# Performance work log

Hardware: AMD Instinct MI355X
Metric: run time of the kernel (lower is better)

The kernel has to match this reference:

```python
import jax, jax.numpy as jnp
from jax import lax
import numpy as np


def setup_inputs() -> dict:
    key = jax.random.key(0)
    ks = jax.random.split(key, 9)
    B, L, Dm = 2, 2048, 768
    di, ds, dc = 1536, 16, 4
    def w(k, shape, fan_in):
        return jax.random.normal(k, shape, jnp.float32) / np.sqrt(fan_in)
    return {
        "x": jax.random.normal(ks[0], (B, L, Dm), jnp.float32),
        "W_in": w(ks[1], (2 * di, Dm), Dm),
        "W_conv": w(ks[2], (di, 1, dc), dc),          # depthwise conv kernel (torch layout)
        "W_x": w(ks[3], (2 * ds, di), di),
        "W_dt": w(ks[4], (di, di), di),
        "b_dt": jax.random.normal(ks[5], (di,), jnp.float32) * 0.1,
        "A_log": jnp.log(jnp.arange(1, ds + 1, dtype=jnp.float32)),
        "D": jnp.ones((di,), jnp.float32),
        "W_out": w(ks[6], (Dm, di), di),
    }


def reference(x, W_in, W_conv, W_x, W_dt, b_dt, A_log, D, W_out):
    B, L, Dm = x.shape
    di = W_in.shape[0] // 2
    ds = A_log.shape[0]
    dc = W_conv.shape[-1]

    xz = x @ W_in.T                                   # (B,L,2*di)
    x_part, z = xz[..., :di], xz[..., di:]

    # causal depthwise conv1d (torch pads dc-1 both sides then truncates -> left pad only)
    xc = lax.conv_general_dilated(
        x_part.transpose(0, 2, 1), W_conv, window_strides=(1,),
        padding=[(dc - 1, 0)], feature_group_count=di)  # (B,di,L)
    xc = jax.nn.silu(xc.transpose(0, 2, 1))            # (B,L,di)

    A = -jnp.exp(A_log)                                # (ds,)
    x_dbl = xc @ W_x.T                                 # (B,L,2*ds)
    B_ssm, C_ssm = x_dbl[..., :ds], x_dbl[..., ds:]
    delta = jax.nn.softplus(xc @ W_dt.T + b_dt)        # (B,L,di)

    deltaA = jnp.exp(delta[..., None] * A)             # (B,L,di,ds)
    deltaB = delta[..., None] * B_ssm[:, :, None, :]   # (B,L,di,ds)

    def step(h, inp):
        dA_t, dB_t, C_t = inp                          # (B,di,ds),(B,di,ds),(B,ds)
        h = dA_t * h + dB_t
        y = jnp.einsum('bds,bs->bd', h, C_t)
        return h, y

    h0 = jnp.zeros((B, di, ds), x.dtype)
    _, ys = lax.scan(step, h0, (deltaA.transpose(1, 0, 2, 3),
                                deltaB.transpose(1, 0, 2, 3),
                                C_ssm.transpose(1, 0, 2)))
    y = ys.transpose(1, 0, 2) + D * xc                 # (B,L,di)
    y = y * jax.nn.silu(z)
    return y @ W_out.T                                 # (B,L,Dm)
```

## Files before the change

### kernel.cpp

```cpp
#include <hip/hip_runtime.h>
#include <hip/hip_bf16.h>

#define BB 2
#define LL 2048
#define DM 768
#define DI 1536
#define DS 16
#define MM (BB*LL)
#define NCH 32
#define CHL 64
#define SEQS (BB*DI*DS)
#define NC2 1664

typedef __hip_bfloat16 bf16;
typedef short bf16x8 __attribute__((ext_vector_type(8)));
typedef float f32x4  __attribute__((ext_vector_type(4)));

__device__ __forceinline__ void gl_lds16(const void* g, void* l) {
  __builtin_amdgcn_global_load_lds((const __attribute__((address_space(1))) void*)g,
                                   (__attribute__((address_space(3))) void*)l, 16, 0, 0);
}

struct bf4 { __hip_bfloat16 a, b, c, d; };
#define PR0 786432
#define PR1 589824
#define PR2 294912
#define PR3 638976
#define PRTOT (PR0+PR1+PR2+PR3)

__global__ __launch_bounds__(256) void prep_k(const float* __restrict__ x,
                                              const float* __restrict__ Win,
                                              const float* __restrict__ Wout,
                                              const float* __restrict__ Wdt,
                                              const float* __restrict__ Wx,
                                              __hip_bfloat16* __restrict__ xbf,
                                              __hip_bfloat16* __restrict__ Winbf,
                                              __hip_bfloat16* __restrict__ Woutbf,
                                              __hip_bfloat16* __restrict__ Wcomb) {
  int i = blockIdx.x * 256 + threadIdx.x;
  if (i >= PRTOT) return;
  float4 v; __hip_bfloat16* dst; int di_;
  if (i < PR0)                    { v = ((const float4*)x)[i];                 dst = xbf;    di_ = i; }
  else if (i < PR0 + PR1)         { di_ = i - PR0; v = ((const float4*)Win)[di_];  dst = Winbf; }
  else if (i < PR0 + PR1 + PR2)   { di_ = i - PR0 - PR1; v = ((const float4*)Wout)[di_]; dst = Woutbf; }
  else {
    di_ = i - PR0 - PR1 - PR2;
    int e = di_ * 4, row = e / DI, colb = e % DI;
    if (row < DI)            v = ((const float4*)Wdt)[di_];
    else if (row < DI + 32)  v = *(const float4*)(Wx + (size_t)(row - DI) * DI + colb);
    else                     v = make_float4(0.f, 0.f, 0.f, 0.f);
    dst = Wcomb;
  }
  bf4 o = { __float2bfloat16(v.x), __float2bfloat16(v.y),
            __float2bfloat16(v.z), __float2bfloat16(v.w) };
  ((bf4*)dst)[di_] = o;
}

template<int EPI, int BM>
__global__ __launch_bounds__(256) void gemm_db(const bf16* __restrict__ A,
                                               const bf16* __restrict__ W,
                                               void* __restrict__ Cv,
                                               void* __restrict__ C2v,
                                               const float* __restrict__ bias,
                                               int M, int N, int K) {
  constexpr int NA  = BM / 64;
  constexpr int NPW = NA + 2;
  __shared__ short sA[3][BM * 32];
  __shared__ short sB[3][128 * 32];
  const int t = threadIdx.x;
  const int m0 = blockIdx.y * BM, n0 = blockIdx.x * 128;
  const int w = t >> 6, lane = t & 63;
  const int wm = (w >> 1) * (BM / 2), wn = (w & 1) * 64;
  const int ga = wm >> 4, gb = wn >> 4;

  f32x4 acc[BM / 32][4] = {};

  const int srow = lane & 15, skoff = (lane >> 4) * 8;
  const bf16* gA[NA]; const bf16* gB[2];
  #pragma unroll
  for (int j = 0; j < NA; j++)
    gA[j] = A + (size_t)(m0 + (w + 4 * j) * 16 + srow) * K + skoff;
  #pragma unroll
  for (int j = 0; j < 2; j++)
    gB[j] = W + (size_t)(n0 + (w + 4 * j) * 16 + srow) * K + skoff;

  #define ISSUE(buf, k0)                                              \
    do {                                                              \
      _Pragma("unroll")                                               \
      for (int j = 0; j < NA; j++)                                    \
        gl_lds16(gA[j] + (k0), &sA[buf][(w + 4 * j) * 512]);          \
      _Pragma("unroll")                                               \
      for (int j = 0; j < 2; j++)                                     \
        gl_lds16(gB[j] + (k0), &sB[buf][(w + 4 * j) * 512]);          \
    } while (0)

  ISSUE(0, 0);
  ISSUE(1, 32);
  int p = 0;
  for (int k0 = 0; k0 < K; k0 += 32) {
    if (k0 + 32 < K) {
      asm volatile("s_waitcnt vmcnt(%0)\n\ts_barrier" :: "n"(NPW) : "memory");
    } else {
      asm volatile("s_waitcnt vmcnt(0)\n\ts_barrier" ::: "memory");
    }
    if (k0 + 64 < K) {
      int nb = p + 2; if (nb >= 3) nb -= 3;
      ISSUE(nb, k0 + 64);
    }
    const bf16x8* fA = (const bf16x8*)sA[p];
    const bf16x8* fB = (const bf16x8*)sB[p];
    bf16x8 af[BM / 32], bfr[4];
    #pragma unroll
    for (int i = 0; i < BM / 32; i++) af[i]  = fA[(ga + i) * 64 + lane];
    #pragma unroll
    for (int j = 0; j < 4; j++)       bfr[j] = fB[(gb + j) * 64 + lane];
    #pragma unroll
    for (int i = 0; i < BM / 32; i++)
      #pragma unroll
      for (int j = 0; j < 4; j++)
        acc[i][j] = __builtin_amdgcn_mfma_f32_16x16x32_bf16(af[i], bfr[j], acc[i][j], 0, 0, 0);
    p++; if (p >= 3) p = 0;
  }
  #undef ISSUE

  const int q = lane >> 4, mm = lane & 15;
  #pragma unroll
  for (int i = 0; i < BM / 32; i++)
    #pragma unroll
    for (int j = 0; j < 4; j++) {
      int r0  = m0 + wm + i * 16 + q * 4;
      int col = n0 + wn + j * 16 + mm;
      #pragma unroll
      for (int r = 0; r < 4; r++) {
        float v = acc[i][j][r];
        if (EPI == 0) {
          ((float*)Cv)[(size_t)(r0 + r) * N + col] = v;
        } else if (EPI == 5) {
          if (col < DI) ((bf16*)Cv) [(size_t)(r0 + r) * DI + col]        = __float2bfloat16(v);
          else          ((bf16*)C2v)[(size_t)(r0 + r) * DI + (col - DI)] = __float2bfloat16(v);
        } else {
          if (col < DI) {
            float vv = v + bias[col];
            vv = (vv > 15.f) ? vv : __logf(1.f + __expf(vv));
            ((bf16*)Cv)[(size_t)(r0 + r) * DI + col] = __float2bfloat16(vv);
          } else if (col < DI + 32) {
            ((float*)C2v)[(size_t)(r0 + r) * 32 + (col - DI)] = v;
          }
        }
      }
    }
}

__global__ __launch_bounds__(256) void conv_silu_k(const bf16* __restrict__ xpart,
                                                   const float* __restrict__ Wc,
                                                   __hip_bfloat16* __restrict__ xcbf) {
  int idx = blockIdx.x * 256 + threadIdx.x;
  if (idx >= MM * DI) return;
  int d = idx % DI;
  int r = idx / DI;
  int l = r & (LL - 1);
  float4 wv = ((const float4*)Wc)[d];
  const bf16* xp = xpart + (size_t)r * DI + d;
  float acc = wv.w * __bfloat162float(xp[0]);
  if (l >= 1) acc += wv.z * __bfloat162float(xp[-(ptrdiff_t)DI]);
  if (l >= 2) acc += wv.y * __bfloat162float(xp[-(ptrdiff_t)(2 * DI)]);
  if (l >= 3) acc += wv.x * __bfloat162float(xp[-(ptrdiff_t)(3 * DI)]);
  float s = acc / (1.f + __expf(-acc));
  xcbf[idx] = __float2bfloat16(s);
}

__global__ __launch_bounds__(64) void scan_part_k(const bf16* __restrict__ delta,
                                                  const float* __restrict__ xdbl,
                                                  const float* __restrict__ A_log,
                                                  float* __restrict__ prodA,
                                                  float* __restrict__ hend) {
  __shared__ float sBC[CHL * 32];
  const int t = threadIdx.x;
  const int dg = blockIdx.x % (DI / 64);
  const int chunk = (blockIdx.x / (DI / 64)) % NCH;
  const int b = blockIdx.x / ((DI / 64) * NCH);
  const int d = dg * 64 + t;

  float a[16];
  #pragma unroll
  for (int s = 0; s < 16; s++) a[s] = -__expf(A_log[s]);

  const float4* src = (const float4*)(xdbl + ((size_t)b * LL + chunk * CHL) * 32);
  #pragma unroll
  for (int k = 0; k < 8; k++) ((float4*)sBC)[t + k * 64] = src[t + k * 64];
  __syncthreads();

  float h[16], p[16];
  #pragma unroll
  for (int s = 0; s < 16; s++) { h[s] = 0.f; p[s] = 1.f; }

  const bf16* dptr = delta + ((size_t)b * LL + chunk * CHL) * DI + d;
  #pragma unroll 2
  for (int i = 0; i < CHL; i++) {
    float dlt = __bfloat162float(dptr[(size_t)i * DI]);
    const float4* bc = (const float4*)(sBC + i * 32);
    float4 B0 = bc[0], B1 = bc[1], B2 = bc[2], B3 = bc[3];
    float Bv[16] = {B0.x,B0.y,B0.z,B0.w, B1.x,B1.y,B1.z,B1.w,
                    B2.x,B2.y,B2.z,B2.w, B3.x,B3.y,B3.z,B3.w};
    #pragma unroll
    for (int s = 0; s < 16; s++) {
      float dA = __expf(dlt * a[s]);
      h[s] = dA * h[s] + dlt * Bv[s];
      p[s] *= dA;
    }
  }
  size_t o = (size_t)chunk * SEQS + ((size_t)b * DI + d) * 16;
  #pragma unroll
  for (int s = 0; s < 16; s += 4) {
    ((float4*)(prodA + o))[s >> 2] = make_float4(p[s], p[s+1], p[s+2], p[s+3]);
    ((float4*)(hend  + o))[s >> 2] = make_float4(h[s], h[s+1], h[s+2], h[s+3]);
  }
}

__global__ __launch_bounds__(64) void scan_comb_k(const float* __restrict__ prodA,
                                                  const float* __restrict__ hend,
                                                  float* __restrict__ hstart) {
  int idx = blockIdx.x * 64 + threadIdx.x;
  float run = 0.f;
  #pragma unroll
  for (int c = 0; c < NCH; c++) {
    size_t o = (size_t)c * SEQS + idx;
    hstart[o] = run;
    run = prodA[o] * run + hend[o];
  }
}

__global__ __launch_bounds__(64) void scan_fin_k(const bf16* __restrict__ delta,
                                                 const float* __restrict__ xdbl,
                                                 const float* __restrict__ A_log,
                                                 const float* __restrict__ Dp,
                                                 const bf16* __restrict__ xcbf,
                                                 const bf16* __restrict__ zbf,
                                                 const float* __restrict__ hstart,
                                                 __hip_bfloat16* __restrict__ ypbf) {
  __shared__ float sBC[CHL * 32];
  const int t = threadIdx.x;
  const int dg = blockIdx.x % (DI / 64);
  const int chunk = (blockIdx.x / (DI / 64)) % NCH;
  const int b = blockIdx.x / ((DI / 64) * NCH);
  const int d = dg * 64 + t;

  float a[16];
  #pragma unroll
  for (int s = 0; s < 16; s++) a[s] = -__expf(A_log[s]);

  const float4* src = (const float4*)(xdbl + ((size_t)b * LL + chunk * CHL) * 32);
  #pragma unroll
  for (int k = 0; k < 8; k++) ((float4*)sBC)[t + k * 64] = src[t + k * 64];
  __syncthreads();

  float h[16];
  size_t o = (size_t)chunk * SEQS + ((size_t)b * DI + d) * 16;
  #pragma unroll
  for (int s = 0; s < 16; s += 4) {
    float4 v = ((const float4*)(hstart + o))[s >> 2];
    h[s] = v.x; h[s+1] = v.y; h[s+2] = v.z; h[s+3] = v.w;
  }
  const float Dv = Dp[d];

  const size_t rbase = (size_t)b * LL + chunk * CHL;
  const bf16* dptr = delta + rbase * DI + d;
  const bf16* xcp  = xcbf  + rbase * DI + d;
  const bf16* zp   = zbf   + rbase * DI + d;
  __hip_bfloat16* yp = ypbf + rbase * DI + d;

  #pragma unroll 2
  for (int i = 0; i < CHL; i++) {
    float dlt = __bfloat162float(dptr[(size_t)i * DI]);
    const float4* bc = (const float4*)(sBC + i * 32);
    float4 B0 = bc[0], B1 = bc[1], B2 = bc[2], B3 = bc[3];
    float4 C0 = bc[4], C1 = bc[5], C2 = bc[6], C3 = bc[7];
    float Bv[16] = {B0.x,B0.y,B0.z,B0.w, B1.x,B1.y,B1.z,B1.w,
                    B2.x,B2.y,B2.z,B2.w, B3.x,B3.y,B3.z,B3.w};
    float Cv[16] = {C0.x,C0.y,C0.z,C0.w, C1.x,C1.y,C1.z,C1.w,
                    C2.x,C2.y,C2.z,C2.w, C3.x,C3.y,C3.z,C3.w};
    float y = 0.f;
    #pragma unroll
    for (int s = 0; s < 16; s++) {
      float dA = __expf(dlt * a[s]);
      h[s] = dA * h[s] + dlt * Bv[s];
      y += h[s] * Cv[s];
    }
    float xcv = __bfloat162float(xcp[(size_t)i * DI]);
    float zv  = __bfloat162float(zp [(size_t)i * DI]);
    float val = (y + Dv * xcv) * (zv / (1.f + __expf(-zv)));
    yp[(size_t)i * DI] = __float2bfloat16(val);
  }
}

extern "C" void kernel_launch(void* const* d_in, const int* in_sizes, int n_in,
                              void* d_out, int out_size, void* d_ws, size_t ws_size,
                              hipStream_t stream) {
  const float* x      = (const float*)d_in[0];
  const float* W_in   = (const float*)d_in[1];
  const float* W_conv = (const float*)d_in[2];
  const float* W_x    = (const float*)d_in[3];
  const float* W_dt   = (const float*)d_in[4];
  const float* b_dt   = (const float*)d_in[5];
  const float* A_log  = (const float*)d_in[6];
  const float* Dp     = (const float*)d_in[7];
  const float* W_out  = (const float*)d_in[8];
  float* out = (float*)d_out;

  char* ws = (char*)d_ws;
  bf16*  xpartbf = (bf16*)(ws + 0);
  bf16*  zbf     = (bf16*)(ws + 12582912);
  bf16*  xbf     = (bf16*)(ws + 25165824);
  bf16*  Winbf   = (bf16*)(ws + 31457280);
  bf16*  xcbf    = (bf16*)(ws + 36175872);
  bf16*  Wcomb   = (bf16*)(ws + 48758784);
  bf16*  deltabf = (bf16*)(ws + 53870592);
  float* xdbl    = (float*)(ws + 66453504);
  bf16*  ypbf    = (bf16*)(ws + 66977792);
  bf16*  Woutbf  = (bf16*)(ws + 79560704);
  float* prodA   = (float*)(ws + 81920000);
  float* hend    = (float*)(ws + 88211456);
  float* hstart  = (float*)(ws + 94502912);

  prep_k<<<(PRTOT + 255) / 256, 256, 0, stream>>>(x, W_in, W_out, W_dt, W_x,
                                                  xbf, Winbf, Woutbf, Wcomb);

  {
    dim3 g(3072 / 128, 4096 / 128);
    gemm_db<5, 128><<<g, 256, 0, stream>>>(xbf, Winbf, xpartbf, zbf, nullptr, MM, 2 * DI, DM);
  }
  conv_silu_k<<<(MM * DI + 255) / 256, 256, 0, stream>>>(xpartbf, W_conv, xcbf);
  {
    dim3 g(NC2 / 128, 4096 / 128);
    gemm_db<6, 128><<<g, 256, 0, stream>>>(xcbf, Wcomb, deltabf, xdbl, b_dt, MM, NC2, DI);
  }
  scan_part_k<<<BB * NCH * (DI / 64), 64, 0, stream>>>(deltabf, xdbl, A_log, prodA, hend);
  scan_comb_k<<<SEQS / 64, 64, 0, stream>>>(prodA, hend, hstart);
  scan_fin_k<<<BB * NCH * (DI / 64), 64, 0, stream>>>(deltabf, xdbl, A_log, Dp, xcbf, zbf,
                                                      hstart, ypbf);
  {
    dim3 g(768 / 128, 4096 / 64);
    gemm_db<0, 64><<<g, 256, 0, stream>>>(ypbf, Woutbf, out, nullptr, nullptr, MM, DM, DI);
  }
}
```

Baseline: 345.9 us.

## Split-K the output GEMM and use shorter scan chunks

Doubles the number of scan chunks (64 chunks of 32 steps), which doubles the blocks in the partial and final scan kernels and shortens each block's serial recurrence. The combine pass gets longer, and its loop unroll is reduced to 4. The output GEMM switches from 64-row tiles to 128-row tiles with split-K over two z-slices. Each slice writes fp32 partials into the reused workspace, and a separate reduction kernel sums them into the output. This trades an extra launch and partial-sum traffic for larger tiles in the final projection, and it also moves the hend/hstart buffers to fit the larger scan state.

```diff
diff --git a/kernel.cpp b/kernel.cpp
--- a/kernel.cpp
+++ b/kernel.cpp
@@ -7,8 +7,8 @@
 #define DI 1536
 #define DS 16
 #define MM (BB*LL)
-#define NCH 32
-#define CHL 64
+#define NCH 64
+#define CHL 32
 #define SEQS (BB*DI*DS)
 #define NC2 1664
 
@@ -62,13 +62,14 @@
                                                void* __restrict__ Cv,
                                                void* __restrict__ C2v,
                                                const float* __restrict__ bias,
-                                               int M, int N, int K) {
+                                               int M, int N, int K, int Kstride) {
   constexpr int NA  = BM / 64;
   constexpr int NPW = NA + 2;
   __shared__ short sA[3][BM * 32];
   __shared__ short sB[3][128 * 32];
   const int t = threadIdx.x;
   const int m0 = blockIdx.y * BM, n0 = blockIdx.x * 128;
+  const size_t koff = (size_t)blockIdx.z * K;
   const int w = t >> 6, lane = t & 63;
   const int wm = (w >> 1) * (BM / 2), wn = (w & 1) * 64;
   const int ga = wm >> 4, gb = wn >> 4;
@@ -79,10 +80,10 @@
   const bf16* gA[NA]; const bf16* gB[2];
   #pragma unroll
   for (int j = 0; j < NA; j++)
-    gA[j] = A + (size_t)(m0 + (w + 4 * j) * 16 + srow) * K + skoff;
+    gA[j] = A + (size_t)(m0 + (w + 4 * j) * 16 + srow) * Kstride + koff + skoff;
   #pragma unroll
   for (int j = 0; j < 2; j++)
-    gB[j] = W + (size_t)(n0 + (w + 4 * j) * 16 + srow) * K + skoff;
+    gB[j] = W + (size_t)(n0 + (w + 4 * j) * 16 + srow) * Kstride + koff + skoff;
 
   #define ISSUE(buf, k0)                                              \
     do {                                                              \
@@ -138,7 +139,7 @@
         } else if (EPI == 5) {
           if (col < DI) ((bf16*)Cv) [(size_t)(r0 + r) * DI + col]        = __float2bfloat16(v);
           else          ((bf16*)C2v)[(size_t)(r0 + r) * DI + (col - DI)] = __float2bfloat16(v);
-        } else {
+        } else if (EPI == 6) {
           if (col < DI) {
             float vv = v + bias[col];
             vv = (vv > 15.f) ? vv : __logf(1.f + __expf(vv));
@@ -146,9 +147,19 @@
           } else if (col < DI + 32) {
             ((float*)C2v)[(size_t)(r0 + r) * 32 + (col - DI)] = v;
           }
+        } else {
+          ((float*)Cv)[(size_t)blockIdx.z * M * N + (size_t)(r0 + r) * N + col] = v;
         }
       }
     }
+}
+
+__global__ __launch_bounds__(256) void redk_k(const float4* __restrict__ P,
+                                              float4* __restrict__ out, int n4) {
+  int i = blockIdx.x * 256 + threadIdx.x;
+  if (i >= n4) return;
+  float4 a = P[i], b = P[i + n4];
+  out[i] = make_float4(a.x + b.x, a.y + b.y, a.z + b.z, a.w + b.w);
 }
 
 __global__ __launch_bounds__(256) void conv_silu_k(const bf16* __restrict__ xpart,
@@ -187,7 +198,7 @@
 
   const float4* src = (const float4*)(xdbl + ((size_t)b * LL + chunk * CHL) * 32);
   #pragma unroll
-  for (int k = 0; k < 8; k++) ((float4*)sBC)[t + k * 64] = src[t + k * 64];
+  for (int k = 0; k < CHL * 32 / 4 / 64; k++) ((float4*)sBC)[t + k * 64] = src[t + k * 64];
   __syncthreads();
 
   float h[16], p[16];
@@ -222,7 +233,7 @@
                                                   float* __restrict__ hstart) {
   int idx = blockIdx.x * 64 + threadIdx.x;
   float run = 0.f;
-  #pragma unroll
+  #pragma unroll 4
   for (int c = 0; c < NCH; c++) {
     size_t o = (size_t)c * SEQS + idx;
     hstart[o] = run;
@@ -251,7 +262,7 @@
 
   const float4* src = (const float4*)(xdbl + ((size_t)b * LL + chunk * CHL) * 32);
   #pragma unroll
-  for (int k = 0; k < 8; k++) ((float4*)sBC)[t + k * 64] = src[t + k * 64];
+  for (int k = 0; k < CHL * 32 / 4 / 64; k++) ((float4*)sBC)[t + k * 64] = src[t + k * 64];
   __syncthreads();
 
   float h[16];
@@ -319,27 +330,32 @@
   bf16*  ypbf    = (bf16*)(ws + 66977792);
   bf16*  Woutbf  = (bf16*)(ws + 79560704);
   float* prodA   = (float*)(ws + 81920000);
-  float* hend    = (float*)(ws + 88211456);
-  float* hstart  = (float*)(ws + 94502912);
+  float* hend    = (float*)(ws + 94502912);
+  float* hstart  = (float*)(ws + 107085824);
+  float* P3      = (float*)(ws + 0);
 
   prep_k<<<(PRTOT + 255) / 256, 256, 0, stream>>>(x, W_in, W_out, W_dt, W_x,
                                                   xbf, Winbf, Woutbf, Wcomb);
 
   {
-    dim3 g(3072 / 128, 4096 / 128);
-    gemm_db<5, 128><<<g, 256, 0, stream>>>(xbf, Winbf, xpartbf, zbf, nullptr, MM, 2 * DI, DM);
+    dim3 g(3072 / 128, 4096 / 128, 1);
+    gemm_db<5, 128><<<g, 256, 0, stream>>>(xbf, Winbf, xpartbf, zbf, nullptr,
+                                           MM, 2 * DI, DM, DM);
   }
   conv_silu_k<<<(MM * DI + 255) / 256, 256, 0, stream>>>(xpartbf, W_conv, xcbf);
   {
-    dim3 g(NC2 / 128, 4096 / 128);
-    gemm_db<6, 128><<<g, 256, 0, stream>>>(xcbf, Wcomb, deltabf, xdbl, b_dt, MM, NC2, DI);
+    dim3 g(NC2 / 128, 4096 / 128, 1);
+    gemm_db<6, 128><<<g, 256, 0, stream>>>(xcbf, Wcomb, deltabf, xdbl, b_dt,
+                                           MM, NC2, DI, DI);
   }
   scan_part_k<<<BB * NCH * (DI / 64), 64, 0, stream>>>(deltabf, xdbl, A_log, prodA, hend);
   scan_comb_k<<<SEQS / 64, 64, 0, stream>>>(prodA, hend, hstart);
   scan_fin_k<<<BB * NCH * (DI / 64), 64, 0, stream>>>(deltabf, xdbl, A_log, Dp, xcbf, zbf,
                                                       hstart, ypbf);
   {
-    dim3 g(768 / 128, 4096 / 64);
-    gemm_db<0, 64><<<g, 256, 0, stream>>>(ypbf, Woutbf, out, nullptr, nullptr, MM, DM, DI);
-  }
-}
+    dim3 g(768 / 128, 4096 / 128, 2);
+    gemm_db<7, 128><<<g, 256, 0, stream>>>(ypbf, Woutbf, P3, nullptr, nullptr,
+                                           MM, DM, DI / 2, DI);
+  }
+  redk_k<<<(786432 + 255) / 256, 256, 0, stream>>>((const float4*)P3, (float4*)out, 786432);
+}
```

New measurement: 336.2 us. 1.03x faster.
